# Performance work log

Hardware: AMD Instinct MI355X
Metric: run time of the kernel (lower is better)

Reference implementation:

```python
import jax, jax.numpy as jnp
import numpy as np

B, CIN, MID, COUT, H, W = 4, 256, 128, 64, 128, 128
WS, HEADS = 8, 8
HD = MID // HEADS          # head dim = 16
N = WS * WS                # tokens per window = 64


def conv2d(x, w, pad=0, groups=1):
    return jax.lax.conv_general_dilated(
        x, w, (1, 1), ((pad, pad), (pad, pad)),
        feature_group_count=groups,
        dimension_numbers=('NCHW', 'OIHW', 'NCHW'))


def bn(x, g, b):  # eval-mode BatchNorm folded to per-channel affine
    return x * g[None, :, None, None] + b[None, :, None, None]


def setup_inputs() -> dict:
    key = jax.random.key(0)
    ks = jax.random.split(key, 32)
    nrm = lambda i, sh, s: jax.random.normal(ks[i], sh, jnp.float32) * s
    return {
        'x': nrm(0, (B, CIN, H, W), 1.0),
        'conv_w': nrm(1, (MID, CIN, 3, 3), 0.03),
        'bn1_g': 1.0 + nrm(2, (MID,), 0.05), 'bn1_b': nrm(3, (MID,), 0.05),
        'qkv_w': nrm(4, (3 * MID, MID, 1, 1), 0.05),
        'loc1_w': nrm(5, (MID, MID, 3, 3), 0.03),
        'loc1_g': 1.0 + nrm(6, (MID,), 0.05), 'loc1_b': nrm(7, (MID,), 0.05),
        'loc2_w': nrm(8, (MID, MID, 1, 1), 0.05),
        'loc2_g': 1.0 + nrm(9, (MID,), 0.05), 'loc2_b': nrm(10, (MID,), 0.05),
        'rel_table': nrm(11, ((2 * WS - 1) ** 2, HEADS), 0.02),
        'cw_w': nrm(12, (1, 2, 7, 7), 0.1),
        'cw_g': 1.0 + nrm(13, (1,), 0.05), 'cw_b': nrm(14, (1,), 0.05),
        'hc_w': nrm(15, (1, 2, 7, 7), 0.1),
        'hc_g': 1.0 + nrm(16, (1,), 0.05), 'hc_b': nrm(17, (1,), 0.05),
        'hw_w': nrm(18, (1, 2, 7, 7), 0.1),
        'hw_g': 1.0 + nrm(19, (1,), 0.05), 'hw_b': nrm(20, (1,), 0.05),
        'proj_dw': nrm(21, (MID, 1, WS, WS), 0.05),
        'proj_g': 1.0 + nrm(22, (MID,), 0.05), 'proj_b': nrm(23, (MID,), 0.05),
        'proj_pw': nrm(24, (MID, MID, 1, 1), 0.05),
        'up_w': nrm(25, (COUT, MID, 3, 3), 0.03),
    }


def _rel_pos_index():
    coords = np.stack(np.meshgrid(np.arange(WS), np.arange(WS), indexing='ij')).reshape(2, -1)
    rel = (coords[:, :, None] - coords[:, None, :]).transpose(1, 2, 0) + (WS - 1)
    return (rel[:, :, 0] * (2 * WS - 1) + rel[:, :, 1]).reshape(-1)  # [N*N]


def reference(x, conv_w, bn1_g, bn1_b, qkv_w, loc1_w, loc1_g, loc1_b,
              loc2_w, loc2_g, loc2_b, rel_table, cw_w, cw_g, cw_b,
              hc_w, hc_g, hc_b, hw_w, hw_g, hw_b,
              proj_dw, proj_g, proj_b, proj_pw, up_w):
    # DecoderBlock: conv -> BN -> ReLU
    h = jax.nn.relu(bn(conv2d(x, conv_w, pad=1), bn1_g, bn1_b))  # [B,MID,H,W]

    # GlobalLocalAttention
    local = bn(conv2d(h, loc2_w), loc2_g, loc2_b) + bn(conv2d(h, loc1_w, pad=1), loc1_g, loc1_b)

    # windowed qkv (H,W divisible by WS, no pad needed)
    hh, ww = H // WS, W // WS
    qkv = conv2d(h, qkv_w)  # [B, 3*MID, H, W]
    qkv = qkv.reshape(B, 3, HEADS, HD, hh, WS, ww, WS)
    qkv = qkv.transpose(1, 0, 4, 6, 2, 5, 7, 3).reshape(3, B * hh * ww, HEADS, N, HD)
    q, k, v = qkv[0], qkv[1], qkv[2]

    dots = jnp.einsum('bhnd,bhmd->bhnm', q, k) * (HD ** -0.5)  # [Bw,HEADS,N,N]
    bias = rel_table[jnp.asarray(_rel_pos_index())].reshape(N, N, HEADS).transpose(2, 0, 1)
    dots = dots + bias[None]

    # TripletAttention on dots treated as (B', C'=HEADS, H'=N, W'=N)
    def gate(t, w, g, b):
        z = jnp.concatenate([t.max(1, keepdims=True), t.mean(1, keepdims=True)], 1)  # ZPool
        return t * jax.nn.sigmoid(bn(conv2d(z, w, pad=3), g, b))

    d1 = gate(dots.transpose(0, 2, 1, 3), cw_w, cw_g, cw_b).transpose(0, 2, 1, 3)
    d2 = gate(dots.transpose(0, 3, 2, 1), hc_w, hc_g, hc_b).transpose(0, 3, 2, 1)
    d3 = gate(dots, hw_w, hw_g, hw_b)
    dots = (d1 + d2 + d3) / 3.0

    attn = jax.nn.softmax(dots, axis=-1)
    o = jnp.einsum('bhnm,bhmd->bhnd', attn, v)
    o = o.reshape(B, hh, ww, HEADS, WS, WS, HD).transpose(0, 3, 6, 1, 4, 2, 5).reshape(B, MID, H, W)

    # avg+max pooled sigmoid gates (kernel==stride==WS//2, exact reshape pooling)
    kp = WS // 2
    aw = o.reshape(B, MID, H // kp, kp, W)
    Fw = jax.nn.sigmoid(aw.mean(3) + aw.max(3))          # [B,MID,H/4,W]
    ah = o.reshape(B, MID, H, W // kp, kp)
    Fh = jax.nn.sigmoid(ah.mean(4) + ah.max(4))          # [B,MID,H,W/4]
    gmat = jnp.einsum('bchk,bckw->bchw', Fh, Fw)         # [B,MID,H,W]

    out = o * gmat + local
    out = jnp.pad(out, ((0, 0), (0, 0), (0, 1), (0, 1)), mode='reflect')  # pad_out
    # SeparableConvBN proj: depthwise k=WS pad=3 -> BN -> 1x1
    out = conv2d(out, proj_dw, pad=3, groups=MID)
    out = conv2d(bn(out, proj_g, proj_b), proj_pw)
    out = out[:, :, :H, :W]

    # upsample: ConvTranspose2d(k=3, s=2, p=1, op=1) as dilated conv
    up = jax.lax.conv_general_dilated(
        out, up_w, (1, 1), ((1, 2), (1, 2)), lhs_dilation=(2, 2),
        dimension_numbers=('NCHW', 'OIHW', 'NCHW'))  # [B,COUT,2H,2W]
    return up
```

## Files before the change

### kernel.cpp

```cpp
#include <hip/hip_runtime.h>
#include <hip/hip_bf16.h>

typedef __hip_bfloat16 bf16;
typedef __attribute__((ext_vector_type(8))) short short8;
typedef __attribute__((ext_vector_type(4))) float f32x4;

#define DEV __device__ __forceinline__
DEV float b2f(bf16 v){ return __bfloat162float(v); }
DEV bf16 f2b(float v){ return __float2bfloat16(v); }
DEV short f2bs(float v){ union{ bf16 b; short s; } u; u.b = __float2bfloat16(v); return u.s; }
DEV float sigm(float x){ return 1.f/(1.f + expf(-x)); }

#define BB 4
#define CIN 256
#define MID 128
#define COUT 64
#define HH 128
#define WW 128
#define WS 8
#define HEADS 8
#define HD 16
#define NTOK 64
#define NWIN 1024

static const size_t OFF_H     = 0;
static const size_t OFF_LOCAL = 33554432;
static const size_t OFF_Q     = 67108864;
static const size_t OFF_K     = 83886080;
static const size_t OFF_V     = 100663296;
static const size_t OFF_DOTS  = 117440512;
static const size_t OFF_Z1    = 184549376;
static const size_t OFF_Z2    = 186646528;
static const size_t OFF_Z3    = 188743680;
static const size_t OFF_G1    = 205520896;
static const size_t OFF_G2    = 207618048;
static const size_t OFF_G3    = 209715200;
static const size_t OFF_HT    = OFF_DOTS + 34078720;

__global__ __launch_bounds__(256) void k_wrep(const float* __restrict__ w, short* __restrict__ w2){
  int i = blockIdx.x*256 + threadIdx.x;
  int ci = i & 255, co = (i >> 8) & 127, kk = i >> 15;
  w2[i] = f2bs(w[(co*256 + ci)*9 + kk]);
}

__global__ void k_xzero(short* __restrict__ xT){
  int t = blockIdx.x*256 + threadIdx.x;
  int ci = t & 255, side = (t >> 8) & 1, row = t >> 9;
  int cpad = side ? 129 : 0;
  xT[((size_t)row*130 + cpad)*256 + ci] = 0;
}

__global__ __launch_bounds__(256) void k_xrep(const float* __restrict__ x, short* __restrict__ xT){
  const int blk = blockIdx.x;
  const int cgrp = blk & 1, cig = (blk >> 1) & 7, r = (blk >> 4) & 127, b = blk >> 11;
  const int c0 = cgrp*64, ci0 = cig*32;
  __shared__ float lds[32][65];
  const int t = threadIdx.x;
  for (int i = t; i < 2048; i += 256){
    int lci = i >> 6, c = i & 63;
    lds[lci][c] = x[((size_t)(b*256 + ci0 + lci)*128 + r)*128 + c0 + c];
  }
  __syncthreads();
  for (int i = t; i < 2048; i += 256){
    int lci = i & 31, cc = i >> 5;
    xT[((size_t)(b*128 + r)*130 + c0 + cc + 1)*256 + ci0 + lci] = f2bs(lds[lci][cc]);
  }
}

__global__ __launch_bounds__(256) void k_conv1m(const short* __restrict__ xT, const short* __restrict__ w2,
      const float* __restrict__ gg, const float* __restrict__ bb, float* __restrict__ h){
  const int blk = blockIdx.x;
  const int b = blk >> 7, y = blk & 127;
  const int t = threadIdx.x, lane = t & 63, wave = t >> 6;
  const int quad = lane >> 4, l15 = lane & 15;
  const int m0 = (wave >> 1)*64, n0 = (wave & 1)*64;
  __shared__ short as[130][32];
  __shared__ short bs[384][32];
  f32x4 acc[4][4];
  #pragma unroll
  for (int i = 0; i < 4; ++i)
    #pragma unroll
    for (int j = 0; j < 4; ++j) acc[i][j] = (f32x4){0.f,0.f,0.f,0.f};
  for (int ky = 0; ky < 3; ++ky){
    int r = y + ky - 1;
    if ((unsigned)r >= 128u) continue;
    const short* xrow = xT + (size_t)(b*128 + r)*130*256;
    const short* wk   = w2 + (size_t)ky*384*256;
    for (int ch = 0; ch < 8; ++ch){
      const int ci0 = ch*32;
      __syncthreads();
      for (int i = t; i < 520; i += 256){
        int col = i >> 2, cg = i & 3;
        *(uint4*)&as[col][cg*8] = *(const uint4*)&xrow[col*256 + ci0 + cg*8];
      }
      for (int i = t; i < 1536; i += 256){
        int rr = i >> 2, cg = i & 3;
        *(uint4*)&bs[rr][cg*8] = *(const uint4*)&wk[rr*256 + ci0 + cg*8];
      }
      __syncthreads();
      #pragma unroll
      for (int kx = 0; kx < 3; ++kx){
        short8 af[4], bf[4];
        #pragma unroll
        for (int mt = 0; mt < 4; ++mt)
          af[mt] = *(const short8*)&as[m0 + mt*16 + l15 + kx][quad*8];
        #pragma unroll
        for (int nt = 0; nt < 4; ++nt)
          bf[nt] = *(const short8*)&bs[kx*128 + n0 + nt*16 + l15][quad*8];
        #pragma unroll
        for (int mt = 0; mt < 4; ++mt)
          #pragma unroll
          for (int nt = 0; nt < 4; ++nt)
            acc[mt][nt] = __builtin_amdgcn_mfma_f32_16x16x32_bf16(af[mt], bf[nt], acc[mt][nt], 0, 0, 0);
      }
    }
  }
  #pragma unroll
  for (int nt = 0; nt < 4; ++nt){
    int co = n0 + nt*16 + l15;
    float g = gg[co], bia = bb[co];
    #pragma unroll
    for (int mt = 0; mt < 4; ++mt){
      int xb = m0 + mt*16 + quad*4;
      float4 o4;
      o4.x = fmaxf(acc[mt][nt][0]*g + bia, 0.f);
      o4.y = fmaxf(acc[mt][nt][1]*g + bia, 0.f);
      o4.z = fmaxf(acc[mt][nt][2]*g + bia, 0.f);
      o4.w = fmaxf(acc[mt][nt][3]*g + bia, 0.f);
      *(float4*)&h[((size_t)(b*128 + co)*128 + y)*128 + xb] = o4;
    }
  }
}

__global__ void k_hzero(short* __restrict__ hT){
  int t = blockIdx.x*256 + threadIdx.x;
  int ci = t & 127, side = (t >> 7) & 1, row = t >> 8;
  int cpad = side ? 129 : 0;
  hT[((size_t)row*130 + cpad)*128 + ci] = 0;
}

__global__ __launch_bounds__(256) void k_hrep(const float* __restrict__ h, short* __restrict__ hT){
  const int blk = blockIdx.x;
  const int cgrp = blk & 1, cig = (blk >> 1) & 3, r = (blk >> 3) & 127, b = blk >> 10;
  const int c0 = cgrp*64, ci0 = cig*32;
  __shared__ float lds[32][65];
  const int t = threadIdx.x;
  for (int i = t; i < 2048; i += 256){
    int lci = i >> 6, c = i & 63;
    lds[lci][c] = h[((size_t)(b*128 + ci0 + lci)*128 + r)*128 + c0 + c];
  }
  __syncthreads();
  for (int i = t; i < 2048; i += 256){
    int lci = i & 31, cc = i >> 5;
    hT[((size_t)(b*128 + r)*130 + c0 + cc + 1)*128 + ci0 + lci] = f2bs(lds[lci][cc]);
  }
}

__global__ __launch_bounds__(256) void k_lwrep(const float* __restrict__ w1, const float* __restrict__ g1,
      const float* __restrict__ w2, const float* __restrict__ g2, short* __restrict__ wloc){
  int i = blockIdx.x*256 + threadIdx.x;
  int ci = i & 127, row = (i >> 7) % 384, ky = i / 49152;
  int kx = row >> 7, co = row & 127;
  float v = w1[(co*128 + ci)*9 + ky*3 + kx] * g1[co];
  if (ky == 1 && kx == 1) v += w2[co*128 + ci] * g2[co];
  wloc[i] = f2bs(v);
}

__global__ __launch_bounds__(256) void k_localm(const short* __restrict__ hT, const short* __restrict__ wloc,
      const float* __restrict__ b1, const float* __restrict__ b2, float* __restrict__ out){
  const int blk = blockIdx.x;
  const int b = blk >> 7, y = blk & 127;
  const int t = threadIdx.x, lane = t & 63, wave = t >> 6;
  const int quad = lane >> 4, l15 = lane & 15;
  const int m0 = (wave >> 1)*64, n0 = (wave & 1)*64;
  __shared__ short as[130][32];
  __shared__ short bs[384][32];
  f32x4 acc[4][4];
  #pragma unroll
  for (int i = 0; i < 4; ++i)
    #pragma unroll
    for (int j = 0; j < 4; ++j) acc[i][j] = (f32x4){0.f,0.f,0.f,0.f};
  for (int ky = 0; ky < 3; ++ky){
    int r = y + ky - 1;
    if ((unsigned)r >= 128u) continue;
    const short* xrow = hT + (size_t)(b*128 + r)*130*128;
    const short* wk   = wloc + (size_t)ky*384*128;
    for (int ch = 0; ch < 4; ++ch){
      const int ci0 = ch*32;
      __syncthreads();
      for (int i = t; i < 520; i += 256){
        int col = i >> 2, cg = i & 3;
        *(uint4*)&as[col][cg*8] = *(const uint4*)&xrow[col*128 + ci0 + cg*8];
      }
      for (int i = t; i < 1536; i += 256){
        int rr = i >> 2, cg = i & 3;
        *(uint4*)&bs[rr][cg*8] = *(const uint4*)&wk[rr*128 + ci0 + cg*8];
      }
      __syncthreads();
      #pragma unroll
      for (int kx = 0; kx < 3; ++kx){
        short8 af[4], bf[4];
        #pragma unroll
        for (int mt = 0; mt < 4; ++mt)
          af[mt] = *(const short8*)&as[m0 + mt*16 + l15 + kx][quad*8];
        #pragma unroll
        for (int nt = 0; nt < 4; ++nt)
          bf[nt] = *(const short8*)&bs[kx*128 + n0 + nt*16 + l15][quad*8];
        #pragma unroll
        for (int mt = 0; mt < 4; ++mt)
          #pragma unroll
          for (int nt = 0; nt < 4; ++nt)
            acc[mt][nt] = __builtin_amdgcn_mfma_f32_16x16x32_bf16(af[mt], bf[nt], acc[mt][nt], 0, 0, 0);
      }
    }
  }
  #pragma unroll
  for (int nt = 0; nt < 4; ++nt){
    int co = n0 + nt*16 + l15;
    float bia = b1[co] + b2[co];
    #pragma unroll
    for (int mt = 0; mt < 4; ++mt){
      int xb = m0 + mt*16 + quad*4;
      float4 o4;
      o4.x = acc[mt][nt][0] + bia;
      o4.y = acc[mt][nt][1] + bia;
      o4.z = acc[mt][nt][2] + bia;
      o4.w = acc[mt][nt][3] + bia;
      *(float4*)&out[((size_t)(b*128 + co)*128 + y)*128 + xb] = o4;
    }
  }
}

__global__ __launch_bounds__(256) void k_wqkvrep(const float* __restrict__ w, short* __restrict__ wqkv){
  int i = blockIdx.x*256 + threadIdx.x;
  wqkv[i] = f2bs(w[i]);
}

__global__ __launch_bounds__(256) void k_qkvm(const short* __restrict__ hT, const short* __restrict__ wqkv,
      bf16* __restrict__ q, bf16* __restrict__ k, bf16* __restrict__ v){
  const int blk = blockIdx.x, ocg = blockIdx.y;
  const int b = blk >> 7, y = blk & 127;
  const int t = threadIdx.x, lane = t & 63, wave = t >> 6;
  const int quad = lane >> 4, l15 = lane & 15;
  const int m0 = (wave >> 1)*64, n0 = (wave & 1)*64;
  __shared__ short as[128][32];
  __shared__ short bs[128][32];
  const short* xrow = hT + ((size_t)(b*128 + y)*130 + 1)*128;
  const short* wk   = wqkv + (size_t)ocg*128*128;
  f32x4 acc[4][4];
  #pragma unroll
  for (int i = 0; i < 4; ++i)
    #pragma unroll
    for (int j = 0; j < 4; ++j) acc[i][j] = (f32x4){0.f,0.f,0.f,0.f};
  for (int ch = 0; ch < 4; ++ch){
    const int ci0 = ch*32;
    __syncthreads();
    for (int i = t; i < 512; i += 256){
      int col = i >> 2, cg = i & 3;
      *(uint4*)&as[col][cg*8] = *(const uint4*)&xrow[col*128 + ci0 + cg*8];
    }
    for (int i = t; i < 512; i += 256){
      int rr = i >> 2, cg = i & 3;
      *(uint4*)&bs[rr][cg*8] = *(const uint4*)&wk[rr*128 + ci0 + cg*8];
    }
    __syncthreads();
    short8 af[4], bf[4];
    #pragma unroll
    for (int mt = 0; mt < 4; ++mt)
      af[mt] = *(const short8*)&as[m0 + mt*16 + l15][quad*8];
    #pragma unroll
    for (int nt = 0; nt < 4; ++nt)
      bf[nt] = *(const short8*)&bs[n0 + nt*16 + l15][quad*8];
    #pragma unroll
    for (int mt = 0; mt < 4; ++mt)
      #pragma unroll
      for (int nt = 0; nt < 4; ++nt)
        acc[mt][nt] = __builtin_amdgcn_mfma_f32_16x16x32_bf16(af[mt], bf[nt], acc[mt][nt], 0, 0, 0);
  }
  bf16* dst = (ocg == 0) ? q : (ocg == 1) ? k : v;
  const int iy = y & 7, hy = y >> 3;
  #pragma unroll
  for (int nt = 0; nt < 4; ++nt){
    int co = n0 + nt*16 + l15;
    int head = co >> 4, d = co & 15;
    #pragma unroll
    for (int mt = 0; mt < 4; ++mt){
      int xb = m0 + mt*16 + quad*4;
      #pragma unroll
      for (int r = 0; r < 4; ++r){
        int x = xb + r;
        int bw = b*256 + hy*16 + (x >> 3);
        int n = iy*8 + (x & 7);
        dst[((size_t)(bw*8+head)*64 + n)*16 + d] = f2b(acc[mt][nt][r]);
      }
    }
  }
}

__global__ __launch_bounds__(256) void k_dots(const bf16* __restrict__ q, const bf16* __restrict__ kk,
      const float* __restrict__ rel, bf16* __restrict__ dots){
  const int bw = blockIdx.x, hd = blockIdx.y;
  __shared__ bf16 qs[64][16], ks[64][16];
  const int t = threadIdx.x;
  const size_t base = (size_t)(bw*8+hd)*1024;
  for (int i = t; i < 1024; i += 256){ qs[i>>4][i&15] = q[base + i]; ks[i>>4][i&15] = kk[base + i]; }
  __syncthreads();
  const int n = t >> 2, jm = t & 3;
  float qr[16];
  #pragma unroll
  for (int d = 0; d < 16; ++d) qr[d] = b2f(qs[n][d]);
  const int ny = n >> 3, nx = n & 7;
  for (int mm = 0; mm < 16; ++mm){
    int m = jm*16 + mm;
    float a = 0.f;
    #pragma unroll
    for (int d = 0; d < 16; ++d) a += qr[d]*b2f(ks[m][d]);
    int my = m >> 3, mx = m & 7;
    int ridx = (ny - my + 7)*15 + (nx - mx + 7);
    float bias = rel[ridx*8 + hd];
    dots[base*4 + (size_t)n*64 + m] = f2b(a*0.25f + bias);
  }
}

__global__ void k_z1(const bf16* __restrict__ dots, bf16* __restrict__ z){
  int t = blockIdx.x*256 + threadIdx.x;
  int bw = t >> 9, r = t & 511; int hd = r >> 6, m = r & 63;
  const bf16* p = dots + (size_t)(bw*8+hd)*4096 + m;
  float mx = -1e30f, sm = 0.f;
  for (int n = 0; n < 64; ++n){ float v = b2f(p[n*64]); mx = fmaxf(mx,v); sm += v; }
  z[(size_t)bw*1024 + hd*64 + m]       = f2b(mx);
  z[(size_t)bw*1024 + 512 + hd*64 + m] = f2b(sm*(1.f/64.f));
}
__global__ void k_z2(const bf16* __restrict__ dots, bf16* __restrict__ z){
  int t = blockIdx.x*256 + threadIdx.x;
  int bw = t >> 9, r = t & 511; int n = r >> 3, hd = r & 7;
  const bf16* p = dots + ((size_t)(bw*8+hd)*64 + n)*64;
  float mx = -1e30f, sm = 0.f;
  for (int m = 0; m < 64; ++m){ float v = b2f(p[m]); mx = fmaxf(mx,v); sm += v; }
  z[(size_t)bw*1024 + n*8 + hd]       = f2b(mx);
  z[(size_t)bw*1024 + 512 + n*8 + hd] = f2b(sm*(1.f/64.f));
}
__global__ void k_z3(const bf16* __restrict__ dots, bf16* __restrict__ z){
  int t = blockIdx.x*256 + threadIdx.x;
  int bw = t >> 12, r = t & 4095;
  const bf16* p = dots + (size_t)bw*32768 + r;
  float mx = -1e30f, sm = 0.f;
  for (int hd = 0; hd < 8; ++hd){ float v = b2f(p[hd*4096]); mx = fmaxf(mx,v); sm += v; }
  z[(size_t)bw*8192 + r]        = f2b(mx);
  z[(size_t)bw*8192 + 4096 + r] = f2b(sm*0.125f);
}

__global__ __launch_bounds__(256) void k_gate(const bf16* __restrict__ z, const float* __restrict__ w,
      const float* __restrict__ gg, const float* __restrict__ bb, float* __restrict__ G, int R, int C){
  __shared__ float wsm[98];
  const int t = threadIdx.x;
  if (t < 98) wsm[t] = w[t];
  __syncthreads();
  const int bw = blockIdx.x;
  int p = blockIdx.y*256 + t; if (p >= R*C) return;
  int y = p / C, x = p - y*C;
  float acc = 0.f;
  for (int c = 0; c < 2; ++c)
    for (int ky = 0; ky < 7; ++ky){
      int iy = y + ky - 3; if ((unsigned)iy >= (unsigned)R) continue;
      for (int kx = 0; kx < 7; ++kx){
        int ix = x + kx - 3; if ((unsigned)ix >= (unsigned)C) continue;
        acc += b2f(z[((size_t)(bw*2+c)*R + iy)*C + ix]) * wsm[c*49 + ky*7 + kx];
      }
    }
  G[(size_t)bw*R*C + p] = sigm(acc*gg[0] + bb[0]);
}

__global__ __launch_bounds__(256) void k_gate3(const bf16* __restrict__ z, const float* __restrict__ w,
      const float* __restrict__ gg, const float* __restrict__ bb, float* __restrict__ G){
  const int bw = blockIdx.x;
  __shared__ float pad[2][70][72];
  __shared__ float wsm[98];
  const int t = threadIdx.x;
  if (t < 98) wsm[t] = w[t];
  for (int i = t; i < 2*70*70; i += 256){
    int c = i / 4900, r = i % 4900;
    int py = r / 70, px = r % 70;
    int y = py - 3, x = px - 3;
    float v = 0.f;
    if ((unsigned)y < 64u && (unsigned)x < 64u)
      v = b2f(z[(size_t)bw*8192 + c*4096 + y*64 + x]);
    pad[c][py][px] = v;
  }
  __syncthreads();
  const int tx = t & 15, ty = t >> 4;
  const int x0 = tx*4, y0 = ty*4;
  float acc[4][4] = {};
  #pragma unroll
  for (int c = 0; c < 2; ++c){
    float wr[49];
    #pragma unroll
    for (int kk = 0; kk < 49; ++kk) wr[kk] = wsm[c*49 + kk];
    #pragma unroll
    for (int iy = 0; iy < 10; ++iy){
      float row[10];
      #pragma unroll
      for (int j = 0; j < 10; ++j) row[j] = pad[c][y0+iy][x0+j];
      #pragma unroll
      for (int dy = 0; dy < 4; ++dy){
        const int ky = iy - dy;
        if (ky < 0 || ky > 6) continue;
        #pragma unroll
        for (int kx = 0; kx < 7; ++kx){
          float wv = wr[ky*7 + kx];
          #pragma unroll
          for (int dx = 0; dx < 4; ++dx)
            acc[dy][dx] += wv * row[dx + kx];
        }
      }
    }
  }
  float g0 = gg[0], b0 = bb[0];
  #pragma unroll
  for (int dy = 0; dy < 4; ++dy){
    float4 o4;
    o4.x = sigm(acc[dy][0]*g0 + b0);
    o4.y = sigm(acc[dy][1]*g0 + b0);
    o4.z = sigm(acc[dy][2]*g0 + b0);
    o4.w = sigm(acc[dy][3]*g0 + b0);
    *(float4*)&G[(size_t)bw*4096 + (y0+dy)*64 + x0] = o4;
  }
}

__global__ __launch_bounds__(256) void k_attn(const bf16* __restrict__ dots, const float* __restrict__ G1,
      const float* __restrict__ G2, const float* __restrict__ G3, const bf16* __restrict__ v,
      float* __restrict__ o){
  const int bw = blockIdx.x, hd = blockIdx.y;
  const int b = bw >> 8, wy = (bw >> 4) & 15, wx = bw & 15;
  __shared__ float attn[64][65];
  __shared__ bf16 vs[64][16];
  __shared__ float invTot[64];
  const int t = threadIdx.x;
  for (int i = t; i < 1024; i += 256) vs[i>>4][i&15] = v[(size_t)(bw*8+hd)*1024 + i];
  const int n = t >> 2, j = t & 3;
  float g2v = G2[(size_t)bw*512 + n*8 + hd];
  const bf16* dp = dots + ((size_t)(bw*8+hd)*64 + n)*64 + j*16;
  const float* g1p = G1 + (size_t)bw*512 + hd*64 + j*16;
  const float* g3p = G3 + (size_t)bw*4096 + n*64 + j*16;
  float e[16]; float mx = -1e30f;
  #pragma unroll
  for (int m = 0; m < 16; ++m){
    float dv = b2f(dp[m]) * ((g1p[m] + g2v + g3p[m]) * (1.f/3.f));
    e[m] = dv; mx = fmaxf(mx, dv);
  }
  mx = fmaxf(mx, __shfl_xor(mx, 1, 4));
  mx = fmaxf(mx, __shfl_xor(mx, 2, 4));
  float s = 0.f;
  #pragma unroll
  for (int m = 0; m < 16; ++m){ float ev = expf(e[m]-mx); e[m] = ev; s += ev; }
  s += __shfl_xor(s, 1, 4);
  s += __shfl_xor(s, 2, 4);
  #pragma unroll
  for (int m = 0; m < 16; ++m) attn[n][j*16+m] = e[m];
  if (j == 0) invTot[n] = 1.f/s;
  __syncthreads();
  const int dg = j;
  float acc[4] = {0.f,0.f,0.f,0.f};
  for (int m = 0; m < 64; ++m){
    float a = attn[n][m];
    #pragma unroll
    for (int dd = 0; dd < 4; ++dd) acc[dd] += a * b2f(vs[m][dg*4+dd]);
  }
  float it = invTot[n];
  int y = wy*8 + (n>>3), x = wx*8 + (n&7);
  #pragma unroll
  for (int dd = 0; dd < 4; ++dd){
    int c = hd*16 + dg*4 + dd;
    o[((size_t)(b*128+c)*128 + y)*128 + x] = acc[dd]*it;
  }
}

__global__ void k_fw(const float* __restrict__ o, float* __restrict__ Fw){
  int t = blockIdx.x*256 + threadIdx.x; if (t >= 4*128*32*128) return;
  int x = t & 127, kk = (t>>7) & 31, bc = t >> 12;
  const float* p = o + ((size_t)bc*128 + kk*4)*128 + x;
  float mx = -1e30f, sm = 0.f;
  #pragma unroll
  for (int r = 0; r < 4; ++r){ float v = p[r*128]; mx = fmaxf(mx,v); sm += v; }
  Fw[t] = sigm(sm*0.25f + mx);
}
__global__ void k_fh(const float* __restrict__ o, float* __restrict__ Fh){
  int t = blockIdx.x*256 + threadIdx.x; if (t >= 4*128*128*32) return;
  int kk = t & 31, y = (t>>5) & 127, bc = t >> 12;
  const float* p = o + ((size_t)bc*128 + y)*128 + kk*4;
  float mx = -1e30f, sm = 0.f;
  #pragma unroll
  for (int r = 0; r < 4; ++r){ float v = p[r]; mx = fmaxf(mx,v); sm += v; }
  Fh[t] = sigm(sm*0.25f + mx);
}

__global__ __launch_bounds__(256) void k_comb(const float* __restrict__ o, const float* __restrict__ Fh,
      const float* __restrict__ Fw, const float* __restrict__ local, float* __restrict__ comb){
  const int bc = blockIdx.x;
  __shared__ float fh[128][33];
  __shared__ float fw[32][129];
  const int t = threadIdx.x;
  for (int i = t; i < 4096; i += 256) fh[i>>5][i&31]  = Fh[(size_t)bc*4096 + i];
  for (int i = t; i < 4096; i += 256) fw[i>>7][i&127] = Fw[(size_t)bc*4096 + i];
  __syncthreads();
  for (int i = t; i < 16384; i += 256){
    int y = i >> 7, x = i & 127;
    float g = 0.f;
    #pragma unroll
    for (int kk = 0; kk < 32; ++kk) g += fh[y][kk]*fw[kk][x];
    size_t idx = (size_t)bc*16384 + i;
    comb[idx] = o[idx]*g + local[idx];
  }
}

__global__ __launch_bounds__(256) void k_dw(const float* __restrict__ comb, const float* __restrict__ dw,
      const float* __restrict__ gg, const float* __restrict__ bb, float* __restrict__ out){
  const int bz = blockIdx.y;
  const int oy0 = blockIdx.x*16;
  const int c = bz & 127;
  __shared__ float xs[23][136];
  __shared__ float wsm[64];
  const int t = threadIdx.x;
  if (t < 64) wsm[t] = dw[c*64 + t];
  for (int i = t; i < 23*135; i += 256){
    int py = i / 135, px = i - py*135;
    int gy = oy0 + py - 3, gx = px - 3;
    float v = 0.f;
    if (gy >= 0 && gy <= 128 && gx >= 0 && gx <= 128){
      int yy = (gy==128)?126:gy, xx = (gx==128)?126:gx;
      v = comb[((size_t)bz*128 + yy)*128 + xx];
    }
    xs[py][px] = v;
  }
  __syncthreads();
  const int tx = t & 31, ty = t >> 5;
  const int x0 = tx*4, y0 = ty*2;
  float acc[2][4] = {};
  #pragma unroll
  for (int iy = 0; iy < 9; ++iy){
    float row[12];
    *(float4*)&row[0] = *(const float4*)&xs[y0+iy][x0];
    *(float4*)&row[4] = *(const float4*)&xs[y0+iy][x0+4];
    *(float4*)&row[8] = *(const float4*)&xs[y0+iy][x0+8];
    #pragma unroll
    for (int dy = 0; dy < 2; ++dy){
      const int ky = iy - dy;
      if (ky < 0 || ky > 7) continue;
      #pragma unroll
      for (int kx = 0; kx < 8; ++kx){
        float wv = wsm[ky*8 + kx];
        #pragma unroll
        for (int dx = 0; dx < 4; ++dx)
          acc[dy][dx] += wv * row[dx + kx];
      }
    }
  }
  float g = gg[c], bi = bb[c];
  #pragma unroll
  for (int dy = 0; dy < 2; ++dy){
    float4 o4;
    o4.x = acc[dy][0]*g + bi;
    o4.y = acc[dy][1]*g + bi;
    o4.z = acc[dy][2]*g + bi;
    o4.w = acc[dy][3]*g + bi;
    *(float4*)&out[((size_t)bz*128 + oy0 + y0 + dy)*128 + x0] = o4;
  }
}

__global__ void k_omzero(short* __restrict__ omT){
  int t = blockIdx.x*256 + threadIdx.x;
  int ci = t & 127, side = (t >> 7) & 1, row = t >> 8;
  int cpad = side ? 129 : 0;
  omT[((size_t)row*130 + cpad)*128 + ci] = 0;
}

__global__ __launch_bounds__(256) void k_uwrep(const float* __restrict__ w, short* __restrict__ wup){
  int i = blockIdx.x*256 + threadIdx.x;
  int ci = i & 127, co = (i >> 7) & 63, tap = i >> 13;
  wup[i] = f2bs(w[(co*128 + ci)*9 + tap]);
}

__global__ __launch_bounds__(256) void k_pw(const float* __restrict__ p1, const float* __restrict__ w,
      short* __restrict__ omT){
  const int pt = blockIdx.x, cb = blockIdx.y;
  const int P0 = pt*64; const int b = P0 >> 14; const int rem0 = P0 & 16383;
  const int y = rem0 >> 7, x0 = rem0 & 127;
  __shared__ float xsm[128][65];
  __shared__ float wsm[64][129];
  const int tx = threadIdx.x, ty = threadIdx.y, t = ty*16+tx;
  for (int i = t; i < 128*64; i += 256){
    int ci = i >> 6, p = i & 63;
    xsm[ci][p] = p1[(size_t)(b*128+ci)*16384 + rem0 + p];
  }
  for (int i = t; i < 64*128; i += 256){
    int co = i >> 7, ci = i & 127;
    wsm[co][ci] = w[(cb*64+co)*128 + ci];
  }
  __syncthreads();
  float acc[4][4] = {};
  for (int ci = 0; ci < 128; ++ci){
    float hv[4], wv[4];
    #pragma unroll
    for (int jj = 0; jj < 4; ++jj) hv[jj] = xsm[ci][jj*16+tx];
    #pragma unroll
    for (int ii = 0; ii < 4; ++ii) wv[ii] = wsm[ii*16+ty][ci];
    #pragma unroll
    for (int ii = 0; ii < 4; ++ii)
      #pragma unroll
      for (int jj = 0; jj < 4; ++jj) acc[ii][jj] += wv[ii]*hv[jj];
  }
  __syncthreads();
  float* pt_t = &xsm[0][0];
  #pragma unroll
  for (int ii = 0; ii < 4; ++ii)
    #pragma unroll
    for (int jj = 0; jj < 4; ++jj)
      pt_t[(jj*16+tx)*65 + ii*16+ty] = acc[ii][jj];
  __syncthreads();
  for (int i = t; i < 4096; i += 256){
    int px = i >> 6, co_l = i & 63;
    omT[((size_t)(b*128 + y)*130 + x0 + px + 1)*128 + cb*64 + co_l] = f2bs(pt_t[px*65 + co_l]);
  }
}

__global__ __launch_bounds__(256) void k_upm(const short* __restrict__ omT, const short* __restrict__ wup,
      float* __restrict__ out){
  const int blk = blockIdx.x;
  const int b = blk >> 7, y = blk & 127;
  const int t = threadIdx.x, lane = t & 63, wave = t >> 6;
  const int quad = lane >> 4, l15 = lane & 15;
  const int m0w = wave*32;
  __shared__ __align__(16) char smem[53504];
  short* asp = (short*)smem;
  short* bsp = (short*)(smem + 16640);
  float* ptile = (float*)smem;
  const int PAR[9] = {3,2,3, 1,0,1, 3,2,3};
  const int ROW[9] = {0,0,0, 0,0,0, 1,1,1};
  const int SHF[9] = {0,0,1, 0,0,1, 0,0,1};
  f32x4 acc[4][2][4];
  #pragma unroll
  for (int p = 0; p < 4; ++p)
    #pragma unroll
    for (int mt = 0; mt < 2; ++mt)
      #pragma unroll
      for (int nt = 0; nt < 4; ++nt) acc[p][mt][nt] = (f32x4){0.f,0.f,0.f,0.f};
  for (int ch = 0; ch < 4; ++ch){
    const int ci0 = ch*32;
    __syncthreads();
    for (int i = t; i < 1040; i += 256){
      int rw = (i >= 520), j = i - rw*520;
      int col = j >> 2, cg = j & 3;
      uint4 val = {0,0,0,0};
      if (y + rw < 128)
        val = *(const uint4*)&omT[((size_t)(b*128 + y + rw)*130 + col)*128 + ci0 + cg*8];
      *(uint4*)&asp[((rw*130 + col)*32) + cg*8] = val;
    }
    for (int i = t; i < 2304; i += 256){
      int rr = i >> 2, cg = i & 3;
      *(uint4*)&bsp[rr*32 + cg*8] = *(const uint4*)&wup[rr*128 + ci0 + cg*8];
    }
    __syncthreads();
    #pragma unroll
    for (int k = 0; k < 9; ++k){
      const int pr = PAR[k], rw = ROW[k], sh = SHF[k];
      if (rw && y == 127) continue;
      short8 af[2], bf[4];
      #pragma unroll
      for (int mt = 0; mt < 2; ++mt)
        af[mt] = *(const short8*)&asp[((rw*130 + m0w + mt*16 + l15 + 1 + sh))*32 + quad*8];
      #pragma unroll
      for (int nt = 0; nt < 4; ++nt)
        bf[nt] = *(const short8*)&bsp[(k*64 + nt*16 + l15)*32 + quad*8];
      #pragma unroll
      for (int mt = 0; mt < 2; ++mt)
        #pragma unroll
        for (int nt = 0; nt < 4; ++nt)
          acc[pr][mt][nt] = __builtin_amdgcn_mfma_f32_16x16x32_bf16(af[mt], bf[nt], acc[pr][mt][nt], 0, 0, 0);
    }
  }
  #pragma unroll
  for (int p = 0; p < 4; ++p){
    __syncthreads();
    #pragma unroll
    for (int mt = 0; mt < 2; ++mt)
      #pragma unroll
      for (int nt = 0; nt < 4; ++nt){
        int co = nt*16 + l15;
        int xb = m0w + mt*16 + quad*4;
        #pragma unroll
        for (int r = 0; r < 4; ++r)
          ptile[co*132 + xb + r] = acc[p][mt][nt][r];
      }
    __syncthreads();
    int py = p >> 1, px = p & 1;
    int Y = 2*y + py;
    for (int i = t; i < 8192; i += 256){
      int co = i >> 7, xx = i & 127;
      out[((size_t)(b*64 + co)*256 + Y)*256 + 2*xx + px] = ptile[co*132 + xx];
    }
  }
}

extern "C" void kernel_launch(void* const* d_in, const int* in_sizes, int n_in,
                              void* d_out, int out_size, void* d_ws, size_t ws_size,
                              hipStream_t stream) {
  const float* x       = (const float*)d_in[0];
  const float* conv_w  = (const float*)d_in[1];
  const float* bn1_g   = (const float*)d_in[2];
  const float* bn1_b   = (const float*)d_in[3];
  const float* qkv_w   = (const float*)d_in[4];
  const float* loc1_w  = (const float*)d_in[5];
  const float* loc1_g  = (const float*)d_in[6];
  const float* loc1_b  = (const float*)d_in[7];
  const float* loc2_w  = (const float*)d_in[8];
  const float* loc2_g  = (const float*)d_in[9];
  const float* loc2_b  = (const float*)d_in[10];
  const float* rel_t   = (const float*)d_in[11];
  const float* cw_w    = (const float*)d_in[12];
  const float* cw_g    = (const float*)d_in[13];
  const float* cw_b    = (const float*)d_in[14];
  const float* hc_w    = (const float*)d_in[15];
  const float* hc_g    = (const float*)d_in[16];
  const float* hc_b    = (const float*)d_in[17];
  const float* hw_w    = (const float*)d_in[18];
  const float* hw_g    = (const float*)d_in[19];
  const float* hw_b    = (const float*)d_in[20];
  const float* proj_dw = (const float*)d_in[21];
  const float* proj_g  = (const float*)d_in[22];
  const float* proj_b  = (const float*)d_in[23];
  const float* proj_pw = (const float*)d_in[24];
  const float* up_w    = (const float*)d_in[25];

  char* ws = (char*)d_ws;
  float* h      = (float*)(ws + OFF_H);
  float* local  = (float*)(ws + OFF_LOCAL);
  bf16*  q      = (bf16*)(ws + OFF_Q);
  bf16*  k      = (bf16*)(ws + OFF_K);
  bf16*  v      = (bf16*)(ws + OFF_V);
  bf16*  dots   = (bf16*)(ws + OFF_DOTS);
  bf16*  z1     = (bf16*)(ws + OFF_Z1);
  bf16*  z2     = (bf16*)(ws + OFF_Z2);
  bf16*  z3     = (bf16*)(ws + OFF_Z3);
  float* G1     = (float*)(ws + OFF_G1);
  float* G2     = (float*)(ws + OFF_G2);
  float* G3     = (float*)(ws + OFF_G3);
  short* xT     = (short*)(ws + OFF_DOTS);
  short* hT     = (short*)(ws + OFF_HT);
  short* w2bf   = (short*)(ws + OFF_Z1);
  short* wloc   = (short*)(ws + OFF_Z2);
  short* wqkv   = (short*)(ws + OFF_Z3);
  short* omT    = (short*)(ws + OFF_DOTS);
  short* wup    = (short*)(ws + OFF_Z1);
  float* o_img  = (float*)(ws + OFF_Q);
  float* Fh     = (float*)(ws + OFF_DOTS);
  float* Fw     = (float*)(ws + OFF_DOTS + 8388608);
  float* comb   = (float*)(ws + OFF_H);
  float* proj1  = (float*)(ws + OFF_LOCAL);
  float* outp   = (float*)d_out;

  dim3 blk2(16,16);
  k_wrep <<<1152, 256, 0, stream>>>(conv_w, w2bf);
  k_xzero<<<1024, 256, 0, stream>>>(xT);
  k_xrep <<<8192, 256, 0, stream>>>(x, xT);
  k_conv1m<<<512, 256, 0, stream>>>(xT, w2bf, bn1_g, bn1_b, h);
  k_lwrep<<<576, 256, 0, stream>>>(loc1_w, loc1_g, loc2_w, loc2_g, wloc);
  k_hzero<<<512, 256, 0, stream>>>(hT);
  k_hrep <<<4096, 256, 0, stream>>>(h, hT);
  k_localm<<<512, 256, 0, stream>>>(hT, wloc, loc1_b, loc2_b, local);
  k_wqkvrep<<<192, 256, 0, stream>>>(qkv_w, wqkv);
  k_qkvm <<<dim3(512,3), 256, 0, stream>>>(hT, wqkv, q, k, v);
  k_dots <<<dim3(NWIN,8), 256, 0, stream>>>(q, k, rel_t, dots);
  k_z1   <<<2048, 256, 0, stream>>>(dots, z1);
  k_z2   <<<2048, 256, 0, stream>>>(dots, z2);
  k_z3   <<<16384, 256, 0, stream>>>(dots, z3);
  k_gate <<<dim3(NWIN,2),  256, 0, stream>>>(z1, cw_w, cw_g, cw_b, G1, 8, 64);
  k_gate <<<dim3(NWIN,2),  256, 0, stream>>>(z2, hc_w, hc_g, hc_b, G2, 64, 8);
  k_gate3<<<NWIN, 256, 0, stream>>>(z3, hw_w, hw_g, hw_b, G3);
  k_attn <<<dim3(NWIN,8), 256, 0, stream>>>(dots, G1, G2, G3, v, o_img);
  k_fw   <<<8192, 256, 0, stream>>>(o_img, Fw);
  k_fh   <<<8192, 256, 0, stream>>>(o_img, Fh);
  k_comb <<<512, 256, 0, stream>>>(o_img, Fh, Fw, local, comb);
  k_dw   <<<dim3(8, BB*128), 256, 0, stream>>>(comb, proj_dw, proj_g, proj_b, proj1);
  k_omzero<<<512, 256, 0, stream>>>(omT);
  k_uwrep<<<288, 256, 0, stream>>>(up_w, wup);
  k_pw   <<<dim3(1024,2), blk2, 0, stream>>>(proj1, proj_pw, omT);
  k_upm  <<<512, 256, 0, stream>>>(omT, wup, outp);
}
```

Before: 723.2 us.

## Fuse conv1 with bf16 transpose, split conv grids, swizzle LDS, merge z reductions

```diff
diff --git a/kernel.cpp b/kernel.cpp
--- a/kernel.cpp
+++ b/kernel.cpp
@@ -9,6 +9,7 @@
 DEV float b2f(bf16 v){ return __bfloat162float(v); }
 DEV bf16 f2b(float v){ return __float2bfloat16(v); }
 DEV short f2bs(float v){ union{ bf16 b; short s; } u; u.b = __float2bfloat16(v); return u.s; }
+DEV float s2f(short s){ union{ short s; bf16 b; } u; u.s = s; return __bfloat162float(u.b); }
 DEV float sigm(float x){ return 1.f/(1.f + expf(-x)); }
 
 #define BB 4
@@ -68,67 +69,76 @@
 }
 
 __global__ __launch_bounds__(256) void k_conv1m(const short* __restrict__ xT, const short* __restrict__ w2,
-      const float* __restrict__ gg, const float* __restrict__ bb, float* __restrict__ h){
+      const float* __restrict__ gg, const float* __restrict__ bb, short* __restrict__ hT){
   const int blk = blockIdx.x;
-  const int b = blk >> 7, y = blk & 127;
+  const int cg = blk & 1, y = (blk >> 1) & 127, b = blk >> 8;
   const int t = threadIdx.x, lane = t & 63, wave = t >> 6;
   const int quad = lane >> 4, l15 = lane & 15;
-  const int m0 = (wave >> 1)*64, n0 = (wave & 1)*64;
-  __shared__ short as[130][32];
-  __shared__ short bs[384][32];
-  f32x4 acc[4][4];
-  #pragma unroll
-  for (int i = 0; i < 4; ++i)
+  const int m0 = wave*32;
+  __shared__ __align__(16) short smem[10304];
+  short (*as)[32] = (short (*)[32])smem;
+  short (*bs)[32] = (short (*)[32])(smem + 4160);
+  f32x4 acc[2][4];
+  #pragma unroll
+  for (int i = 0; i < 2; ++i)
     #pragma unroll
     for (int j = 0; j < 4; ++j) acc[i][j] = (f32x4){0.f,0.f,0.f,0.f};
   for (int ky = 0; ky < 3; ++ky){
     int r = y + ky - 1;
     if ((unsigned)r >= 128u) continue;
     const short* xrow = xT + (size_t)(b*128 + r)*130*256;
-    const short* wk   = w2 + (size_t)ky*384*256;
+    const short* wk   = w2 + (size_t)(ky*384 + cg*64)*256;
     for (int ch = 0; ch < 8; ++ch){
       const int ci0 = ch*32;
       __syncthreads();
       for (int i = t; i < 520; i += 256){
-        int col = i >> 2, cg = i & 3;
-        *(uint4*)&as[col][cg*8] = *(const uint4*)&xrow[col*256 + ci0 + cg*8];
-      }
-      for (int i = t; i < 1536; i += 256){
-        int rr = i >> 2, cg = i & 3;
-        *(uint4*)&bs[rr][cg*8] = *(const uint4*)&wk[rr*256 + ci0 + cg*8];
+        int col = i >> 2, cq = i & 3;
+        *(uint4*)&as[col][(cq ^ (col & 3))*8] = *(const uint4*)&xrow[col*256 + ci0 + cq*8];
+      }
+      for (int i = t; i < 768; i += 256){
+        int rr = i >> 2, cq = i & 3;
+        *(uint4*)&bs[rr][(cq ^ (rr & 3))*8] = *(const uint4*)&wk[(((rr >> 6)<<7) + (rr & 63))*256 + ci0 + cq*8];
       }
       __syncthreads();
       #pragma unroll
       for (int kx = 0; kx < 3; ++kx){
-        short8 af[4], bf[4];
-        #pragma unroll
-        for (int mt = 0; mt < 4; ++mt)
-          af[mt] = *(const short8*)&as[m0 + mt*16 + l15 + kx][quad*8];
-        #pragma unroll
-        for (int nt = 0; nt < 4; ++nt)
-          bf[nt] = *(const short8*)&bs[kx*128 + n0 + nt*16 + l15][quad*8];
-        #pragma unroll
-        for (int mt = 0; mt < 4; ++mt)
+        short8 af[2], bf[4];
+        #pragma unroll
+        for (int mt = 0; mt < 2; ++mt){
+          int row = m0 + mt*16 + l15 + kx;
+          af[mt] = *(const short8*)&as[row][((row & 3) ^ quad)*8];
+        }
+        #pragma unroll
+        for (int nt = 0; nt < 4; ++nt){
+          int row = kx*64 + nt*16 + l15;
+          bf[nt] = *(const short8*)&bs[row][((row & 3) ^ quad)*8];
+        }
+        #pragma unroll
+        for (int mt = 0; mt < 2; ++mt)
           #pragma unroll
           for (int nt = 0; nt < 4; ++nt)
             acc[mt][nt] = __builtin_amdgcn_mfma_f32_16x16x32_bf16(af[mt], bf[nt], acc[mt][nt], 0, 0, 0);
       }
     }
   }
+  __syncthreads();
+  short* tb = smem;
   #pragma unroll
   for (int nt = 0; nt < 4; ++nt){
-    int co = n0 + nt*16 + l15;
+    int cl = nt*16 + l15, co = cg*64 + cl;
     float g = gg[co], bia = bb[co];
     #pragma unroll
-    for (int mt = 0; mt < 4; ++mt){
+    for (int mt = 0; mt < 2; ++mt){
       int xb = m0 + mt*16 + quad*4;
-      float4 o4;
-      o4.x = fmaxf(acc[mt][nt][0]*g + bia, 0.f);
-      o4.y = fmaxf(acc[mt][nt][1]*g + bia, 0.f);
-      o4.z = fmaxf(acc[mt][nt][2]*g + bia, 0.f);
-      o4.w = fmaxf(acc[mt][nt][3]*g + bia, 0.f);
-      *(float4*)&h[((size_t)(b*128 + co)*128 + y)*128 + xb] = o4;
-    }
+      #pragma unroll
+      for (int r2 = 0; r2 < 4; ++r2)
+        tb[(xb + r2)*72 + cl] = f2bs(fmaxf(acc[mt][nt][r2]*g + bia, 0.f));
+    }
+  }
+  __syncthreads();
+  for (int i = t; i < 1024; i += 256){
+    int xx = i >> 3, c8 = i & 7;
+    *(uint4*)&hT[((size_t)(b*128 + y)*130 + xx + 1)*128 + cg*64 + c8*8] = *(const uint4*)&tb[xx*72 + c8*8];
   }
 }
 
@@ -137,23 +147,6 @@
   int ci = t & 127, side = (t >> 7) & 1, row = t >> 8;
   int cpad = side ? 129 : 0;
   hT[((size_t)row*130 + cpad)*128 + ci] = 0;
-}
-
-__global__ __launch_bounds__(256) void k_hrep(const float* __restrict__ h, short* __restrict__ hT){
-  const int blk = blockIdx.x;
-  const int cgrp = blk & 1, cig = (blk >> 1) & 3, r = (blk >> 3) & 127, b = blk >> 10;
-  const int c0 = cgrp*64, ci0 = cig*32;
-  __shared__ float lds[32][65];
-  const int t = threadIdx.x;
-  for (int i = t; i < 2048; i += 256){
-    int lci = i >> 6, c = i & 63;
-    lds[lci][c] = h[((size_t)(b*128 + ci0 + lci)*128 + r)*128 + c0 + c];
-  }
-  __syncthreads();
-  for (int i = t; i < 2048; i += 256){
-    int lci = i & 31, cc = i >> 5;
-    hT[((size_t)(b*128 + r)*130 + c0 + cc + 1)*128 + ci0 + lci] = f2bs(lds[lci][cc]);
-  }
 }
 
 __global__ __launch_bounds__(256) void k_lwrep(const float* __restrict__ w1, const float* __restrict__ g1,
@@ -169,45 +162,49 @@
 __global__ __launch_bounds__(256) void k_localm(const short* __restrict__ hT, const short* __restrict__ wloc,
       const float* __restrict__ b1, const float* __restrict__ b2, float* __restrict__ out){
   const int blk = blockIdx.x;
-  const int b = blk >> 7, y = blk & 127;
+  const int cg = blk & 1, y = (blk >> 1) & 127, b = blk >> 8;
   const int t = threadIdx.x, lane = t & 63, wave = t >> 6;
   const int quad = lane >> 4, l15 = lane & 15;
-  const int m0 = (wave >> 1)*64, n0 = (wave & 1)*64;
+  const int m0 = wave*32;
   __shared__ short as[130][32];
-  __shared__ short bs[384][32];
-  f32x4 acc[4][4];
-  #pragma unroll
-  for (int i = 0; i < 4; ++i)
+  __shared__ short bs[192][32];
+  f32x4 acc[2][4];
+  #pragma unroll
+  for (int i = 0; i < 2; ++i)
     #pragma unroll
     for (int j = 0; j < 4; ++j) acc[i][j] = (f32x4){0.f,0.f,0.f,0.f};
   for (int ky = 0; ky < 3; ++ky){
     int r = y + ky - 1;
     if ((unsigned)r >= 128u) continue;
     const short* xrow = hT + (size_t)(b*128 + r)*130*128;
-    const short* wk   = wloc + (size_t)ky*384*128;
+    const short* wk   = wloc + (size_t)(ky*384 + cg*64)*128;
     for (int ch = 0; ch < 4; ++ch){
       const int ci0 = ch*32;
       __syncthreads();
       for (int i = t; i < 520; i += 256){
-        int col = i >> 2, cg = i & 3;
-        *(uint4*)&as[col][cg*8] = *(const uint4*)&xrow[col*128 + ci0 + cg*8];
-      }
-      for (int i = t; i < 1536; i += 256){
-        int rr = i >> 2, cg = i & 3;
-        *(uint4*)&bs[rr][cg*8] = *(const uint4*)&wk[rr*128 + ci0 + cg*8];
+        int col = i >> 2, cq = i & 3;
+        *(uint4*)&as[col][(cq ^ (col & 3))*8] = *(const uint4*)&xrow[col*128 + ci0 + cq*8];
+      }
+      for (int i = t; i < 768; i += 256){
+        int rr = i >> 2, cq = i & 3;
+        *(uint4*)&bs[rr][(cq ^ (rr & 3))*8] = *(const uint4*)&wk[(((rr >> 6)<<7) + (rr & 63))*128 + ci0 + cq*8];
       }
       __syncthreads();
       #pragma unroll
       for (int kx = 0; kx < 3; ++kx){
-        short8 af[4], bf[4];
-        #pragma unroll
-        for (int mt = 0; mt < 4; ++mt)
-          af[mt] = *(const short8*)&as[m0 + mt*16 + l15 + kx][quad*8];
-        #pragma unroll
-        for (int nt = 0; nt < 4; ++nt)
-          bf[nt] = *(const short8*)&bs[kx*128 + n0 + nt*16 + l15][quad*8];
-        #pragma unroll
-        for (int mt = 0; mt < 4; ++mt)
+        short8 af[2], bf[4];
+        #pragma unroll
+        for (int mt = 0; mt < 2; ++mt){
+          int row = m0 + mt*16 + l15 + kx;
+          af[mt] = *(const short8*)&as[row][((row & 3) ^ quad)*8];
+        }
+        #pragma unroll
+        for (int nt = 0; nt < 4; ++nt){
+          int row = kx*64 + nt*16 + l15;
+          bf[nt] = *(const short8*)&bs[row][((row & 3) ^ quad)*8];
+        }
+        #pragma unroll
+        for (int mt = 0; mt < 2; ++mt)
           #pragma unroll
           for (int nt = 0; nt < 4; ++nt)
             acc[mt][nt] = __builtin_amdgcn_mfma_f32_16x16x32_bf16(af[mt], bf[nt], acc[mt][nt], 0, 0, 0);
@@ -216,10 +213,10 @@
   }
   #pragma unroll
   for (int nt = 0; nt < 4; ++nt){
-    int co = n0 + nt*16 + l15;
+    int co = cg*64 + nt*16 + l15;
     float bia = b1[co] + b2[co];
     #pragma unroll
-    for (int mt = 0; mt < 4; ++mt){
+    for (int mt = 0; mt < 2; ++mt){
       int xb = m0 + mt*16 + quad*4;
       float4 o4;
       o4.x = acc[mt][nt][0] + bia;
@@ -256,21 +253,25 @@
     const int ci0 = ch*32;
     __syncthreads();
     for (int i = t; i < 512; i += 256){
-      int col = i >> 2, cg = i & 3;
-      *(uint4*)&as[col][cg*8] = *(const uint4*)&xrow[col*128 + ci0 + cg*8];
+      int col = i >> 2, cq = i & 3;
+      *(uint4*)&as[col][(cq ^ (col & 3))*8] = *(const uint4*)&xrow[col*128 + ci0 + cq*8];
     }
     for (int i = t; i < 512; i += 256){
-      int rr = i >> 2, cg = i & 3;
-      *(uint4*)&bs[rr][cg*8] = *(const uint4*)&wk[rr*128 + ci0 + cg*8];
+      int rr = i >> 2, cq = i & 3;
+      *(uint4*)&bs[rr][(cq ^ (rr & 3))*8] = *(const uint4*)&wk[rr*128 + ci0 + cq*8];
     }
     __syncthreads();
     short8 af[4], bf[4];
     #pragma unroll
-    for (int mt = 0; mt < 4; ++mt)
-      af[mt] = *(const short8*)&as[m0 + mt*16 + l15][quad*8];
-    #pragma unroll
-    for (int nt = 0; nt < 4; ++nt)
-      bf[nt] = *(const short8*)&bs[n0 + nt*16 + l15][quad*8];
+    for (int mt = 0; mt < 4; ++mt){
+      int row = m0 + mt*16 + l15;
+      af[mt] = *(const short8*)&as[row][((row & 3) ^ quad)*8];
+    }
+    #pragma unroll
+    for (int nt = 0; nt < 4; ++nt){
+      int row = n0 + nt*16 + l15;
+      bf[nt] = *(const short8*)&bs[row][((row & 3) ^ quad)*8];
+    }
     #pragma unroll
     for (int mt = 0; mt < 4; ++mt)
       #pragma unroll
@@ -322,32 +323,71 @@
   }
 }
 
-__global__ void k_z1(const bf16* __restrict__ dots, bf16* __restrict__ z){
-  int t = blockIdx.x*256 + threadIdx.x;
-  int bw = t >> 9, r = t & 511; int hd = r >> 6, m = r & 63;
-  const bf16* p = dots + (size_t)(bw*8+hd)*4096 + m;
-  float mx = -1e30f, sm = 0.f;
-  for (int n = 0; n < 64; ++n){ float v = b2f(p[n*64]); mx = fmaxf(mx,v); sm += v; }
-  z[(size_t)bw*1024 + hd*64 + m]       = f2b(mx);
-  z[(size_t)bw*1024 + 512 + hd*64 + m] = f2b(sm*(1.f/64.f));
-}
-__global__ void k_z2(const bf16* __restrict__ dots, bf16* __restrict__ z){
-  int t = blockIdx.x*256 + threadIdx.x;
-  int bw = t >> 9, r = t & 511; int n = r >> 3, hd = r & 7;
-  const bf16* p = dots + ((size_t)(bw*8+hd)*64 + n)*64;
-  float mx = -1e30f, sm = 0.f;
-  for (int m = 0; m < 64; ++m){ float v = b2f(p[m]); mx = fmaxf(mx,v); sm += v; }
-  z[(size_t)bw*1024 + n*8 + hd]       = f2b(mx);
-  z[(size_t)bw*1024 + 512 + n*8 + hd] = f2b(sm*(1.f/64.f));
-}
-__global__ void k_z3(const bf16* __restrict__ dots, bf16* __restrict__ z){
-  int t = blockIdx.x*256 + threadIdx.x;
-  int bw = t >> 12, r = t & 4095;
-  const bf16* p = dots + (size_t)bw*32768 + r;
-  float mx = -1e30f, sm = 0.f;
-  for (int hd = 0; hd < 8; ++hd){ float v = b2f(p[hd*4096]); mx = fmaxf(mx,v); sm += v; }
-  z[(size_t)bw*8192 + r]        = f2b(mx);
-  z[(size_t)bw*8192 + 4096 + r] = f2b(sm*0.125f);
+__global__ __launch_bounds__(256) void k_zall(const bf16* __restrict__ dots,
+      bf16* __restrict__ z1, bf16* __restrict__ z2, bf16* __restrict__ z3){
+  const int bw = blockIdx.x;
+  const int t = threadIdx.x;
+  const int q4 = t >> 2, j4 = t & 3;
+  __shared__ float sd[64][65];
+  float mx3[16], sm3[16];
+  #pragma unroll
+  for (int i = 0; i < 16; ++i){ mx3[i] = -1e30f; sm3[i] = 0.f; }
+  const short* dp = (const short*)dots + (size_t)bw*32768;
+  for (int hd = 0; hd < 8; ++hd){
+    __syncthreads();
+    const short* p = dp + (size_t)hd*4096;
+    #pragma unroll
+    for (int g = 0; g < 2; ++g){
+      short8 s8 = *(const short8*)&p[t*16 + g*8];
+      #pragma unroll
+      for (int j = 0; j < 8; ++j){
+        float vv = s2f(s8[j]);
+        sd[q4][j4*16 + g*8 + j] = vv;
+        mx3[g*8+j] = fmaxf(mx3[g*8+j], vv);
+        sm3[g*8+j] += vv;
+      }
+    }
+    __syncthreads();
+    float mx = -1e30f, sm = 0.f;
+    #pragma unroll
+    for (int m = 0; m < 16; ++m){
+      float vv = sd[q4][j4*16 + m];
+      mx = fmaxf(mx, vv); sm += vv;
+    }
+    mx = fmaxf(mx, __shfl_xor(mx, 1, 4));
+    mx = fmaxf(mx, __shfl_xor(mx, 2, 4));
+    sm += __shfl_xor(sm, 1, 4);
+    sm += __shfl_xor(sm, 2, 4);
+    if (j4 == 0){
+      z2[(size_t)bw*1024 + q4*8 + hd]       = f2b(mx);
+      z2[(size_t)bw*1024 + 512 + q4*8 + hd] = f2b(sm*(1.f/64.f));
+    }
+    float mxc = -1e30f, smc = 0.f;
+    #pragma unroll
+    for (int nn = 0; nn < 16; ++nn){
+      float vv = sd[j4*16 + nn][q4];
+      mxc = fmaxf(mxc, vv); smc += vv;
+    }
+    mxc = fmaxf(mxc, __shfl_xor(mxc, 1, 4));
+    mxc = fmaxf(mxc, __shfl_xor(mxc, 2, 4));
+    smc += __shfl_xor(smc, 1, 4);
+    smc += __shfl_xor(smc, 2, 4);
+    if (j4 == 0){
+      z1[(size_t)bw*1024 + hd*64 + q4]       = f2b(mxc);
+      z1[(size_t)bw*1024 + 512 + hd*64 + q4] = f2b(smc*(1.f/64.f));
+    }
+  }
+  short* zp = (short*)z3 + (size_t)bw*8192;
+  short8 o0, o1, p0, p1;
+  #pragma unroll
+  for (int j = 0; j < 8; ++j){
+    o0[j] = f2bs(mx3[j]);        o1[j] = f2bs(mx3[8+j]);
+    p0[j] = f2bs(sm3[j]*0.125f); p1[j] = f2bs(sm3[8+j]*0.125f);
+  }
+  *(short8*)&zp[t*16]          = o0;
+  *(short8*)&zp[t*16 + 8]      = o1;
+  *(short8*)&zp[4096 + t*16]   = p0;
+  *(short8*)&zp[4096 + t*16+8] = p1;
 }
 
 __global__ __launch_bounds__(256) void k_gate(const bf16* __restrict__ z, const float* __restrict__ w,
@@ -649,15 +689,16 @@
     __syncthreads();
     for (int i = t; i < 1040; i += 256){
       int rw = (i >= 520), j = i - rw*520;
-      int col = j >> 2, cg = j & 3;
+      int col = j >> 2, cq = j & 3;
+      int row = rw*130 + col;
       uint4 val = {0,0,0,0};
       if (y + rw < 128)
-        val = *(const uint4*)&omT[((size_t)(b*128 + y + rw)*130 + col)*128 + ci0 + cg*8];
-      *(uint4*)&asp[((rw*130 + col)*32) + cg*8] = val;
+        val = *(const uint4*)&omT[((size_t)(b*128 + y + rw)*130 + col)*128 + ci0 + cq*8];
+      *(uint4*)&asp[row*32 + (cq ^ (row & 3))*8] = val;
     }
     for (int i = t; i < 2304; i += 256){
-      int rr = i >> 2, cg = i & 3;
-      *(uint4*)&bsp[rr*32 + cg*8] = *(const uint4*)&wup[rr*128 + ci0 + cg*8];
+      int rr = i >> 2, cq = i & 3;
+      *(uint4*)&bsp[rr*32 + (cq ^ (rr & 3))*8] = *(const uint4*)&wup[rr*128 + ci0 + cq*8];
     }
     __syncthreads();
     #pragma unroll
@@ -666,11 +707,15 @@
       if (rw && y == 127) continue;
       short8 af[2], bf[4];
       #pragma unroll
-      for (int mt = 0; mt < 2; ++mt)
-        af[mt] = *(const short8*)&asp[((rw*130 + m0w + mt*16 + l15 + 1 + sh))*32 + quad*8];
-      #pragma unroll
-      for (int nt = 0; nt < 4; ++nt)
-        bf[nt] = *(const short8*)&bsp[(k*64 + nt*16 + l15)*32 + quad*8];
+      for (int mt = 0; mt < 2; ++mt){
+        int row = rw*130 + m0w + mt*16 + l15 + 1 + sh;
+        af[mt] = *(const short8*)&asp[row*32 + ((row & 3) ^ quad)*8];
+      }
+      #pragma unroll
+      for (int nt = 0; nt < 4; ++nt){
+        int row = k*64 + nt*16 + l15;
+        bf[nt] = *(const short8*)&bsp[row*32 + ((row & 3) ^ quad)*8];
+      }
       #pragma unroll
       for (int mt = 0; mt < 2; ++mt)
         #pragma unroll
@@ -732,7 +777,6 @@
   const float* up_w    = (const float*)d_in[25];
 
   char* ws = (char*)d_ws;
-  float* h      = (float*)(ws + OFF_H);
   float* local  = (float*)(ws + OFF_LOCAL);
   bf16*  q      = (bf16*)(ws + OFF_Q);
   bf16*  k      = (bf16*)(ws + OFF_K);
@@ -762,17 +806,14 @@
   k_wrep <<<1152, 256, 0, stream>>>(conv_w, w2bf);
   k_xzero<<<1024, 256, 0, stream>>>(xT);
   k_xrep <<<8192, 256, 0, stream>>>(x, xT);
-  k_conv1m<<<512, 256, 0, stream>>>(xT, w2bf, bn1_g, bn1_b, h);
+  k_hzero<<<512, 256, 0, stream>>>(hT);
+  k_conv1m<<<1024, 256, 0, stream>>>(xT, w2bf, bn1_g, bn1_b, hT);
   k_lwrep<<<576, 256, 0, stream>>>(loc1_w, loc1_g, loc2_w, loc2_g, wloc);
-  k_hzero<<<512, 256, 0, stream>>>(hT);
-  k_hrep <<<4096, 256, 0, stream>>>(h, hT);
-  k_localm<<<512, 256, 0, stream>>>(hT, wloc, loc1_b, loc2_b, local);
+  k_localm<<<1024, 256, 0, stream>>>(hT, wloc, loc1_b, loc2_b, local);
   k_wqkvrep<<<192, 256, 0, stream>>>(qkv_w, wqkv);
   k_qkvm <<<dim3(512,3), 256, 0, stream>>>(hT, wqkv, q, k, v);
   k_dots <<<dim3(NWIN,8), 256, 0, stream>>>(q, k, rel_t, dots);
-  k_z1   <<<2048, 256, 0, stream>>>(dots, z1);
-  k_z2   <<<2048, 256, 0, stream>>>(dots, z2);
-  k_z3   <<<16384, 256, 0, stream>>>(dots, z3);
+  k_zall <<<NWIN, 256, 0, stream>>>(dots, z1, z2, z3);
   k_gate <<<dim3(NWIN,2),  256, 0, stream>>>(z1, cw_w, cw_g, cw_b, G1, 8, 64);
   k_gate <<<dim3(NWIN,2),  256, 0, stream>>>(z2, hc_w, hc_g, hc_b, G2, 64, 8);
   k_gate3<<<NWIN, 256, 0, stream>>>(z3, hw_w, hw_g, hw_b, G3);
```

Result: faster. 657.5 us (-9.1%).
